# Optimization experiments

Hardware: AMD Instinct MI355X
Metric: run time of the kernel (lower is better)

## Reference

```python
import jax, jax.numpy as jnp
import numpy as np

N, E = 50000, 800000
IN, HID, H1, H2, OUT = 128, 64, 4, 6, 121
NEG_SLOPE = 0.2


def setup_inputs() -> dict:
    key = jax.random.key(0)
    ks = jax.random.split(key, 16)
    s = 0.1  # weight init scale
    return {
        "x": jax.random.normal(ks[0], (N, IN), jnp.float32),
        "src": jax.random.randint(ks[1], (E,), 0, N),
        "dst": jax.random.randint(ks[2], (E,), 0, N),
        # conv1: in=IN, heads=H1, out=HID, concat
        "W1": jax.random.normal(ks[3], (IN, H1 * HID), jnp.float32) * s,
        "a1_src": jax.random.normal(ks[4], (H1, HID), jnp.float32) * s,
        "a1_dst": jax.random.normal(ks[5], (H1, HID), jnp.float32) * s,
        "b1": jnp.zeros((H1 * HID,), jnp.float32),
        # conv2: in=H1*HID, heads=H1, out=HID, concat, residual
        "W2": jax.random.normal(ks[6], (H1 * HID, H1 * HID), jnp.float32) * s,
        "a2_src": jax.random.normal(ks[7], (H1, HID), jnp.float32) * s,
        "a2_dst": jax.random.normal(ks[8], (H1, HID), jnp.float32) * s,
        "b2": jnp.zeros((H1 * HID,), jnp.float32),
        "Wres2": jax.random.normal(ks[9], (H1 * HID, H1 * HID), jnp.float32) * s,
        # conv3: in=H1*HID, heads=H2, out=OUT, mean (concat=False)
        "W3": jax.random.normal(ks[10], (H1 * HID, H2 * OUT), jnp.float32) * s,
        "a3_src": jax.random.normal(ks[11], (H2, OUT), jnp.float32) * s,
        "a3_dst": jax.random.normal(ks[12], (H2, OUT), jnp.float32) * s,
        "b3": jnp.zeros((OUT,), jnp.float32),
    }


def _segment_softmax(e, seg, n):
    # e: [E, H], softmax over edges sharing the same destination node
    m = jax.ops.segment_max(e, seg, num_segments=n)
    ex = jnp.exp(e - m[seg])
    s = jax.ops.segment_sum(ex, seg, num_segments=n)
    return ex / (s[seg] + 1e-16)


def _gat_conv(x, src, dst, W, a_src, a_dst, b, heads, ch, concat, Wres=None):
    n = x.shape[0]
    h = (x @ W).reshape(n, heads, ch)                       # [N, H, C]
    al_s = jnp.sum(h * a_src, axis=-1)                      # [N, H]
    al_d = jnp.sum(h * a_dst, axis=-1)                      # [N, H]
    e = jax.nn.leaky_relu(al_s[src] + al_d[dst], NEG_SLOPE)  # [E, H]
    alpha = _segment_softmax(e, dst, n)                     # [E, H]
    msg = h[src] * alpha[..., None]                         # [E, H, C]
    out = jax.ops.segment_sum(msg, dst, num_segments=n)     # [N, H, C]
    out = out.reshape(n, heads * ch) if concat else out.mean(axis=1)
    if Wres is not None:
        out = out + x @ Wres
    return out + b


def reference(x, src, dst, W1, a1_src, a1_dst, b1, W2, a2_src, a2_dst, b2,
              Wres2, W3, a3_src, a3_dst, b3):
    n = x.shape[0]
    # PyG GATConv default: add self-loops
    loop = jnp.arange(n, dtype=src.dtype)
    s = jnp.concatenate([src, loop])
    d = jnp.concatenate([dst, loop])
    h = jax.nn.elu(_gat_conv(x, s, d, W1, a1_src, a1_dst, b1, H1, HID, True))
    h = jax.nn.elu(_gat_conv(h, s, d, W2, a2_src, a2_dst, b2, H1, HID, True, Wres=Wres2))
    h = _gat_conv(h, s, d, W3, a3_src, a3_dst, b3, H2, OUT, False)
    return jax.nn.sigmoid(h)
```

## Files before the change

kernel.cpp:

```cpp
#include <hip/hip_runtime.h>
#include <hip/hip_bf16.h>


#define NODES 50000
#define EDGES 800000
#define MPAD  50048
#define C0    25088
#define C1    24912

typedef unsigned short u16;
typedef __attribute__((ext_vector_type(8))) short bf16x8;
typedef __attribute__((ext_vector_type(4))) float f32x4;

__device__ __forceinline__ float bf16f(u16 r) {
    return __uint_as_float(((unsigned)r) << 16);
}
__device__ __forceinline__ u16 f2b(float v) {
    __hip_bfloat16 b = __float2bfloat16(v);
    return *(u16*)&b;
}
__device__ __forceinline__ float blo(unsigned d) { return __uint_as_float(d << 16); }
__device__ __forceinline__ float bhi(unsigned d) { return __uint_as_float(d & 0xffff0000u); }


__global__ void fill_ones_kernel(int* __restrict__ deg, int n) {
    int i = blockIdx.x * blockDim.x + threadIdx.x;
    if (i < n) deg[i] = 1;
}

__global__ void hist_kernel(const int* __restrict__ dst, int* __restrict__ deg, int E) {
    int e = blockIdx.x * blockDim.x + threadIdx.x;
    if (e < E) atomicAdd(&deg[dst[e]], 1);
}

__global__ void deg_bsum_kernel(const int* __restrict__ deg, int* __restrict__ bsum, int n) {
    int tid = threadIdx.x, lane = tid & 63, wid = tid >> 6;
    int i = blockIdx.x * 256 + tid;
    int v = (i < n) ? deg[i] : 0;
    #pragma unroll
    for (int ofs = 32; ofs > 0; ofs >>= 1) v += __shfl_down(v, ofs);
    __shared__ int sp[4];
    if (lane == 0) sp[wid] = v;
    __syncthreads();
    if (tid == 0) bsum[blockIdx.x] = sp[0] + sp[1] + sp[2] + sp[3];
}

__global__ void bsum_scan_kernel(int* __restrict__ bsum, int* __restrict__ row_ptr,
                                 int nb, int n) {
    int tid = threadIdx.x, lane = tid & 63, wid = tid >> 6;
    int v = (tid < nb) ? bsum[tid] : 0;
    int incl = v;
    #pragma unroll
    for (int ofs = 1; ofs < 64; ofs <<= 1) {
        int t = __shfl_up(incl, ofs);
        if (lane >= ofs) incl += t;
    }
    __shared__ int sp[4];
    if (lane == 63) sp[wid] = incl;
    __syncthreads();
    int add = 0;
    for (int k = 0; k < wid; k++) add += sp[k];
    int excl = incl - v + add;
    if (tid < nb) bsum[tid] = excl;
    if (tid == nb - 1) row_ptr[n] = excl + v;
}

__global__ void deg_scan_kernel(const int* __restrict__ deg, const int* __restrict__ bofs,
                                int* __restrict__ row_ptr, int* __restrict__ cursor, int n) {
    int tid = threadIdx.x, lane = tid & 63, wid = tid >> 6;
    int i = blockIdx.x * 256 + tid;
    int v = (i < n) ? deg[i] : 0;
    int incl = v;
    #pragma unroll
    for (int ofs = 1; ofs < 64; ofs <<= 1) {
        int t = __shfl_up(incl, ofs);
        if (lane >= ofs) incl += t;
    }
    __shared__ int sp[4];
    if (lane == 63) sp[wid] = incl;
    __syncthreads();
    int add = bofs[blockIdx.x];
    for (int k = 0; k < wid; k++) add += sp[k];
    int excl = incl - v + add;
    if (i < n) { row_ptr[i] = excl; cursor[i] = excl; }
}

__global__ void scatter_kernel(const int* __restrict__ src, const int* __restrict__ dst,
                               int E, int n, int* __restrict__ cursor, int* __restrict__ csr_src) {
    int e = blockIdx.x * blockDim.x + threadIdx.x;
    if (e < E) {
        int d = dst[e];
        int p = atomicAdd(&cursor[d], 1);
        csr_src[p] = src[e];
    } else if (e < E + n) {
        int i = e - E;
        int p = atomicAdd(&cursor[i], 1);
        csr_src[p] = i;
    }
}


__global__ void prep_weights(
    const float* __restrict__ W1, const float* __restrict__ W2,
    const float* __restrict__ Wres2, const float* __restrict__ W3,
    const float* __restrict__ a1s, const float* __restrict__ a1d,
    const float* __restrict__ a2s, const float* __restrict__ a2d,
    const float* __restrict__ a3s, const float* __restrict__ a3d,
    u16* __restrict__ WT1, u16* __restrict__ WT2, u16* __restrict__ W3sT,
    float* __restrict__ q1t, float* __restrict__ q2t, float* __restrict__ cm) {
    int idx = blockIdx.x * 256 + threadIdx.x;
    if (idx < 32768) {
        int n = idx >> 7, k = idx & 127;
        WT1[idx] = f2b(W1[(size_t)k * 256 + n]);
    } else if ((idx -= 32768) < 131072) {
        int n = idx >> 8, k = idx & 255;
        float v = (n < 256) ? W2[(size_t)k * 256 + n] : Wres2[(size_t)k * 256 + (n - 256)];
        WT2[idx] = f2b(v);
    } else if ((idx -= 131072) < 196608) {
        int n = idx / 1536, q = idx % 1536;
        int h = q >> 8, k = q & 255;
        W3sT[idx] = f2b((n < 121) ? W3[(size_t)k * 726 + h * 121 + n] : 0.f);
    } else if ((idx -= 196608) < 1024) {
        int h = idx >> 7, k = idx & 127;
        int hh = h & 3;
        const float* a = (h < 4) ? a1s : a1d;
        float v = 0.f;
        for (int c = 0; c < 64; c++) v += W1[(size_t)k * 256 + hh * 64 + c] * a[hh * 64 + c];
        q1t[idx] = v;
    } else if ((idx -= 1024) < 2048) {
        int h = idx >> 8, k = idx & 255;
        int hh = h & 3;
        const float* a = (h < 4) ? a2s : a2d;
        float v = 0.f;
        for (int c = 0; c < 64; c++) v += W2[(size_t)k * 256 + hh * 64 + c] * a[hh * 64 + c];
        q2t[idx] = v;
    } else if ((idx -= 2048) < 3072) {
        int o = idx >> 8, k = idx & 255;
        int h = (o < 6) ? o : o - 6;
        const float* a = (o < 6) ? a3s : a3d;
        float v = 0.f;
        for (int c = 0; c < 121; c++) v += W3[(size_t)k * 726 + h * 121 + c] * a[h * 121 + c];
        cm[idx] = v;
    }
}
#define PREP_TOTAL (32768 + 131072 + 196608 + 1024 + 2048 + 3072)


__global__ __launch_bounds__(256) void convx_al1(
    const float* __restrict__ x, const float* __restrict__ q1t,
    u16* __restrict__ A2a, float* __restrict__ alA, int n) {
    int wid = threadIdx.x >> 6, lane = threadIdx.x & 63;
    int i = blockIdx.x * 4 + wid;
    if (i >= n) return;
    float2 xv = *(const float2*)(x + (size_t)i * 128 + lane * 2);
    ushort2 o;
    o.x = f2b(xv.x); o.y = f2b(xv.y);
    *(ushort2*)(A2a + (size_t)i * 128 + lane * 2) = o;
    float p[8];
    #pragma unroll
    for (int h = 0; h < 8; h++) {
        float2 q = *(const float2*)(q1t + h * 128 + lane * 2);
        p[h] = xv.x * q.x + xv.y * q.y;
    }
    #pragma unroll
    for (int ofs = 1; ofs <= 32; ofs <<= 1) {
        #pragma unroll
        for (int h = 0; h < 8; h++) p[h] += __shfl_xor(p[h], ofs);
    }
    if (lane == 0) {
        *(float4*)(alA + (size_t)i * 8)     = make_float4(p[0], p[1], p[2], p[3]);
        *(float4*)(alA + (size_t)i * 8 + 4) = make_float4(p[4], p[5], p[6], p[7]);
    }
}


__global__ __launch_bounds__(256) void row_logit8(
    const u16* __restrict__ f, const float* __restrict__ q,
    float* __restrict__ al, int n) {
    int wid = threadIdx.x >> 6, lane = threadIdx.x & 63;
    int i = blockIdx.x * 4 + wid;
    if (i >= n) return;
    uint2 d = *(const uint2*)(f + (size_t)i * 256 + lane * 4);
    float v0 = blo(d.x), v1 = bhi(d.x), v2 = blo(d.y), v3 = bhi(d.y);
    float p[8];
    #pragma unroll
    for (int h = 0; h < 8; h++) {
        float4 c = *(const float4*)(q + (size_t)h * 256 + lane * 4);
        p[h] = v0 * c.x + v1 * c.y + v2 * c.z + v3 * c.w;
    }
    #pragma unroll
    for (int ofs = 1; ofs <= 32; ofs <<= 1) {
        #pragma unroll
        for (int h = 0; h < 8; h++) p[h] += __shfl_xor(p[h], ofs);
    }
    if (lane == 0) {
        *(float4*)(al + (size_t)i * 8)     = make_float4(p[0], p[1], p[2], p[3]);
        *(float4*)(al + (size_t)i * 8 + 4) = make_float4(p[4], p[5], p[6], p[7]);
    }
}

__global__ __launch_bounds__(256) void row_logit12(
    const u16* __restrict__ f, const float* __restrict__ q,
    float* __restrict__ al, int n) {
    int wid = threadIdx.x >> 6, lane = threadIdx.x & 63;
    int i = blockIdx.x * 4 + wid;
    if (i >= n) return;
    uint2 d = *(const uint2*)(f + (size_t)i * 256 + lane * 4);
    float v0 = blo(d.x), v1 = bhi(d.x), v2 = blo(d.y), v3 = bhi(d.y);
    float p[12];
    #pragma unroll
    for (int h = 0; h < 12; h++) {
        float4 c = *(const float4*)(q + (size_t)h * 256 + lane * 4);
        p[h] = v0 * c.x + v1 * c.y + v2 * c.z + v3 * c.w;
    }
    #pragma unroll
    for (int ofs = 1; ofs <= 32; ofs <<= 1) {
        #pragma unroll
        for (int h = 0; h < 12; h++) p[h] += __shfl_xor(p[h], ofs);
    }
    if (lane == 0) {
        *(float4*)(al + (size_t)i * 12)     = make_float4(p[0], p[1], p[2], p[3]);
        *(float4*)(al + (size_t)i * 12 + 4) = make_float4(p[4], p[5], p[6], p[7]);
        *(float4*)(al + (size_t)i * 12 + 8) = make_float4(p[8], p[9], p[10], p[11]);
    }
}


__global__ __launch_bounds__(256) void gemm_mfma_kernel(
    const u16* __restrict__ A, const u16* __restrict__ B,
    u16* __restrict__ Cb, u16* __restrict__ Cb2,
    int M, int Ncols, int K2, int ldc, int split) {
    __shared__ __align__(16) u16 As[128][40];
    __shared__ __align__(16) u16 Bs[128][40];
    int tid = threadIdx.x;
    int lane = tid & 63;
    int wv = tid >> 6;
    int quad = lane >> 4, lm = lane & 15;
    int wm = (wv & 1) * 64, wn = (wv >> 1) * 64;
    int bm = blockIdx.x * 128, bn = blockIdx.y * 128;

    f32x4 zero = {0.f, 0.f, 0.f, 0.f};
    f32x4 acc[4][4];
    #pragma unroll
    for (int i = 0; i < 4; i++)
        #pragma unroll
        for (int j = 0; j < 4; j++) acc[i][j] = zero;

    for (int k0 = 0; k0 < K2; k0 += 32) {
        #pragma unroll
        for (int it = 0; it < 2; ++it) {
            int chunk = tid + it * 256;
            int row = chunk >> 2, seg = chunk & 3;
            uint4 va = *(const uint4*)(A + (size_t)(bm + row) * K2 + k0 + seg * 8);
            uint4 vb = *(const uint4*)(B + (size_t)(bn + row) * K2 + k0 + seg * 8);
            *(uint4*)&As[row][seg * 8] = va;
            *(uint4*)&Bs[row][seg * 8] = vb;
        }
        __syncthreads();
        bf16x8 af[4], bfr[4];
        #pragma unroll
        for (int i = 0; i < 4; i++) af[i] = *(const bf16x8*)&As[wm + i * 16 + lm][quad * 8];
        #pragma unroll
        for (int j = 0; j < 4; j++) bfr[j] = *(const bf16x8*)&Bs[wn + j * 16 + lm][quad * 8];
        #pragma unroll
        for (int i = 0; i < 4; i++)
            #pragma unroll
            for (int j = 0; j < 4; j++)
                acc[i][j] = __builtin_amdgcn_mfma_f32_16x16x32_bf16(af[i], bfr[j], acc[i][j], 0, 0, 0);
        __syncthreads();
    }

    #pragma unroll
    for (int i = 0; i < 4; i++) {
        #pragma unroll
        for (int j = 0; j < 4; j++) {
            int col = bn + wn + j * 16 + lm;
            if (col >= Ncols) continue;
            int row_base = bm + wm + i * 16 + quad * 4;
            #pragma unroll
            for (int r = 0; r < 4; r++) {
                int row = row_base + r;
                if (row >= M) continue;
                float v = acc[i][j][r];
                if (col < split) Cb[(size_t)row * ldc + col] = f2b(v);
                else             Cb2[(size_t)row * ldc + col - split] = f2b(v);
            }
        }
    }
}


__global__ __launch_bounds__(256) void gemm_skinny64(
    const u16* __restrict__ A, const u16* __restrict__ B,
    float* __restrict__ C, const float* __restrict__ bias, int count) {
    __shared__ __align__(16) u16 As[64][40];
    __shared__ __align__(16) u16 Bs[128][40];
    int tid = threadIdx.x, lane = tid & 63, wv = tid >> 6;
    int quad = lane >> 4, lm = lane & 15;
    int bm = blockIdx.x * 64;
    int mrow = (wv >> 1) * 32, ncol = (wv & 1) * 64;
    int ar = bm + (tid >> 2);
    if (ar >= count) ar = count - 1;
    const u16* Ap = A + (size_t)ar * 1536 + (tid & 3) * 8;

    f32x4 zero = {0.f, 0.f, 0.f, 0.f};
    f32x4 acc[2][4];
    #pragma unroll
    for (int i = 0; i < 2; i++)
        #pragma unroll
        for (int j = 0; j < 4; j++) acc[i][j] = zero;

    for (int k0 = 0; k0 < 1536; k0 += 32) {
        *(uint4*)&As[tid >> 2][(tid & 3) * 8] = *(const uint4*)(Ap + k0);
        #pragma unroll
        for (int it = 0; it < 2; ++it) {
            int t = tid + it * 256;
            *(uint4*)&Bs[t >> 2][(t & 3) * 8] =
                *(const uint4*)(B + (size_t)(t >> 2) * 1536 + k0 + (t & 3) * 8);
        }
        __syncthreads();
        bf16x8 af[2], bfr[4];
        #pragma unroll
        for (int i = 0; i < 2; i++) af[i] = *(const bf16x8*)&As[mrow + i * 16 + lm][quad * 8];
        #pragma unroll
        for (int j = 0; j < 4; j++) bfr[j] = *(const bf16x8*)&Bs[ncol + j * 16 + lm][quad * 8];
        #pragma unroll
        for (int i = 0; i < 2; i++)
            #pragma unroll
            for (int j = 0; j < 4; j++)
                acc[i][j] = __builtin_amdgcn_mfma_f32_16x16x32_bf16(af[i], bfr[j], acc[i][j], 0, 0, 0);
        __syncthreads();
    }

    #pragma unroll
    for (int i = 0; i < 2; i++) {
        #pragma unroll
        for (int j = 0; j < 4; j++) {
            int col = ncol + j * 16 + lm;
            if (col >= 121) continue;
            int row_base = bm + mrow + i * 16 + quad * 4;
            #pragma unroll
            for (int r = 0; r < 4; r++) {
                int row = row_base + r;
                if (row >= count) continue;
                float v = acc[i][j][r] + bias[col];
                v = 1.f / (1.f + __expf(-v));
                C[(size_t)row * 121 + col] = v;
            }
        }
    }
}


#define ACC8(wt, dv) \
    acc[0] = fmaf(wt, blo(dv.x), acc[0]); acc[1] = fmaf(wt, bhi(dv.x), acc[1]); \
    acc[2] = fmaf(wt, blo(dv.y), acc[2]); acc[3] = fmaf(wt, bhi(dv.y), acc[3]); \
    acc[4] = fmaf(wt, blo(dv.z), acc[4]); acc[5] = fmaf(wt, bhi(dv.z), acc[5]); \
    acc[6] = fmaf(wt, blo(dv.w), acc[6]); acc[7] = fmaf(wt, bhi(dv.w), acc[7]);

__global__ __launch_bounds__(256) void agg4_fused(
    const u16* __restrict__ f, const float* __restrict__ al8,
    const int* __restrict__ row_ptr, const int* __restrict__ csr_src,
    const float* __restrict__ bias, const u16* __restrict__ resb,
    u16* __restrict__ outb, int n) {
    int wid = threadIdx.x >> 6, lane = threadIdx.x & 63;
    int i = blockIdx.x * 4 + wid;
    if (i >= n) return;
    int beg = row_ptr[i], end = row_ptr[i + 1];
    int h_st = lane >> 4;
    int el = lane & 15;
    int half = lane >> 5;
    int c8 = (lane & 31) * 8;
    int wsel = (lane & 24) << 1;
    float ald_st = al8[(size_t)i * 8 + 4 + h_st];
    float acc[8] = {};
    float S = 0.f;
    for (int base = beg; base < end; base += 16) {
        int cnt = min(16, end - base);
        int idxv = csr_src[base + min(el, cnt - 1)];
        float av = al8[(size_t)idxv * 8 + h_st] + ald_st;
        av = av > 0.f ? av : 0.2f * av;
        float ex = __expf(fminf(av, 60.f));
        int e = 0;
        for (; e + 8 <= cnt; e += 8) {
            int s0 = __shfl(idxv, e + half);
            int s1 = __shfl(idxv, e + 2 + half);
            int s2 = __shfl(idxv, e + 4 + half);
            int s3 = __shfl(idxv, e + 6 + half);
            uint4 d0 = *(const uint4*)(f + (size_t)s0 * 256 + c8);
            uint4 d1 = *(const uint4*)(f + (size_t)s1 * 256 + c8);
            uint4 d2 = *(const uint4*)(f + (size_t)s2 * 256 + c8);
            uint4 d3 = *(const uint4*)(f + (size_t)s3 * 256 + c8);
            float w0 = __shfl(ex, wsel | (e + half));
            float w1 = __shfl(ex, wsel | (e + 2 + half));
            float w2 = __shfl(ex, wsel | (e + 4 + half));
            float w3 = __shfl(ex, wsel | (e + 6 + half));
            S += (w0 + w1) + (w2 + w3);
            ACC8(w0, d0);
            ACC8(w1, d1);
            ACC8(w2, d2);
            ACC8(w3, d3);
        }
        for (; e + 4 <= cnt; e += 4) {
            int s0 = __shfl(idxv, e + half);
            int s1 = __shfl(idxv, e + 2 + half);
            uint4 d0 = *(const uint4*)(f + (size_t)s0 * 256 + c8);
            uint4 d1 = *(const uint4*)(f + (size_t)s1 * 256 + c8);
            float w0 = __shfl(ex, wsel | (e + half));
            float w1 = __shfl(ex, wsel | (e + 2 + half));
            S += w0 + w1;
            ACC8(w0, d0);
            ACC8(w1, d1);
        }
        for (; e < cnt; e += 2) {
            int ei = e + half;
            int eu = ei < cnt ? ei : e;
            int s = __shfl(idxv, eu);
            float w = __shfl(ex, wsel | eu);
            if (ei >= cnt) w = 0.f;
            S += w;
            uint4 d = *(const uint4*)(f + (size_t)s * 256 + c8);
            ACC8(w, d);
        }
    }
    #pragma unroll
    for (int k = 0; k < 8; k++) acc[k] += __shfl_xor(acc[k], 32);
    S += __shfl_xor(S, 32);
    if (half == 0) {
        float inv = 1.f / (S + 1e-16f);
        float4 b0 = *(const float4*)(bias + c8);
        float4 b1 = *(const float4*)(bias + c8 + 4);
        float v[8];
        v[0] = acc[0] * inv + b0.x; v[1] = acc[1] * inv + b0.y;
        v[2] = acc[2] * inv + b0.z; v[3] = acc[3] * inv + b0.w;
        v[4] = acc[4] * inv + b1.x; v[5] = acc[5] * inv + b1.y;
        v[6] = acc[6] * inv + b1.z; v[7] = acc[7] * inv + b1.w;
        if (resb) {
            uint4 r = *(const uint4*)(resb + (size_t)i * 256 + c8);
            v[0] += blo(r.x); v[1] += bhi(r.x); v[2] += blo(r.y); v[3] += bhi(r.y);
            v[4] += blo(r.z); v[5] += bhi(r.z); v[6] += blo(r.w); v[7] += bhi(r.w);
        }
        #pragma unroll
        for (int k = 0; k < 8; k++) v[k] = v[k] > 0.f ? v[k] : (__expf(v[k]) - 1.f);
        uint4 o;
        o.x = (unsigned)f2b(v[0]) | ((unsigned)f2b(v[1]) << 16);
        o.y = (unsigned)f2b(v[2]) | ((unsigned)f2b(v[3]) << 16);
        o.z = (unsigned)f2b(v[4]) | ((unsigned)f2b(v[5]) << 16);
        o.w = (unsigned)f2b(v[6]) | ((unsigned)f2b(v[7]) << 16);
        *(uint4*)(outb + (size_t)i * 256 + c8) = o;
    }
}


__global__ __launch_bounds__(256) void aggS_fused(
    const u16* __restrict__ x, const float* __restrict__ al3,
    const int* __restrict__ row_ptr, const int* __restrict__ csr_src,
    u16* __restrict__ S, int node0, int count) {
    __shared__ int s_i[4][16];
    __shared__ float s_w[4][96];
    int wid = threadIdx.x >> 6, lane = threadIdx.x & 63;
    int li = blockIdx.x * 4 + wid;
    if (li >= count) return;
    int i = node0 + li;
    int beg = row_ptr[i], end = row_ptr[i + 1];
    int c4 = lane * 4;
    int e16 = lane & 15;
    int hA = lane >> 4;
    int hB = 4 + (lane >> 4);
    float aldA = al3[(size_t)i * 12 + 6 + hA];
    float aldB = (lane < 32) ? al3[(size_t)i * 12 + 6 + hB] : 0.f;
    float acc[6][4] = {};
    float Ssum[6] = {};
    for (int base = beg; base < end; base += 16) {
        int cnt = min(16, end - base);
        int idxe = csr_src[base + min(e16, cnt - 1)];
        if (lane < 16) s_i[wid][lane] = idxe;
        float vA = al3[(size_t)idxe * 12 + hA] + aldA;
        vA = vA > 0.f ? vA : 0.2f * vA;
        float exA = __expf(fminf(vA, 60.f));
        if (e16 < cnt) s_w[wid][e16 * 6 + hA] = exA;
        if (lane < 32) {
            float vB = al3[(size_t)idxe * 12 + hB] + aldB;
            vB = vB > 0.f ? vB : 0.2f * vB;
            float exB = __expf(fminf(vB, 60.f));
            if (e16 < cnt) s_w[wid][e16 * 6 + hB] = exB;
        }
        int e = 0;
        for (; e + 4 <= cnt; e += 4) {
            int s0 = s_i[wid][e],     s1 = s_i[wid][e + 1];
            int s2 = s_i[wid][e + 2], s3 = s_i[wid][e + 3];
            uint2 d0 = *(const uint2*)(x + (size_t)s0 * 256 + c4);
            uint2 d1 = *(const uint2*)(x + (size_t)s1 * 256 + c4);
            uint2 d2 = *(const uint2*)(x + (size_t)s2 * 256 + c4);
            uint2 d3 = *(const uint2*)(x + (size_t)s3 * 256 + c4);
            float f00 = blo(d0.x), f01 = bhi(d0.x), f02 = blo(d0.y), f03 = bhi(d0.y);
            float f10 = blo(d1.x), f11 = bhi(d1.x), f12 = blo(d1.y), f13 = bhi(d1.y);
            float f20 = blo(d2.x), f21 = bhi(d2.x), f22 = blo(d2.y), f23 = bhi(d2.y);
            float f30 = blo(d3.x), f31 = bhi(d3.x), f32 = blo(d3.y), f33 = bhi(d3.y);
            #pragma unroll
            for (int hh = 0; hh < 6; hh++) {
                float w0 = s_w[wid][e * 6 + hh];
                float w1 = s_w[wid][(e + 1) * 6 + hh];
                float w2 = s_w[wid][(e + 2) * 6 + hh];
                float w3 = s_w[wid][(e + 3) * 6 + hh];
                Ssum[hh] += (w0 + w1) + (w2 + w3);
                acc[hh][0] = fmaf(w0, f00, acc[hh][0]);
                acc[hh][1] = fmaf(w0, f01, acc[hh][1]);
                acc[hh][2] = fmaf(w0, f02, acc[hh][2]);
                acc[hh][3] = fmaf(w0, f03, acc[hh][3]);
                acc[hh][0] = fmaf(w1, f10, acc[hh][0]);
                acc[hh][1] = fmaf(w1, f11, acc[hh][1]);
                acc[hh][2] = fmaf(w1, f12, acc[hh][2]);
                acc[hh][3] = fmaf(w1, f13, acc[hh][3]);
                acc[hh][0] = fmaf(w2, f20, acc[hh][0]);
                acc[hh][1] = fmaf(w2, f21, acc[hh][1]);
                acc[hh][2] = fmaf(w2, f22, acc[hh][2]);
                acc[hh][3] = fmaf(w2, f23, acc[hh][3]);
                acc[hh][0] = fmaf(w3, f30, acc[hh][0]);
                acc[hh][1] = fmaf(w3, f31, acc[hh][1]);
                acc[hh][2] = fmaf(w3, f32, acc[hh][2]);
                acc[hh][3] = fmaf(w3, f33, acc[hh][3]);
            }
        }
        for (; e < cnt; e++) {
            int s = s_i[wid][e];
            uint2 d = *(const uint2*)(x + (size_t)s * 256 + c4);
            float v0 = blo(d.x), v1 = bhi(d.x), v2 = blo(d.y), v3 = bhi(d.y);
            #pragma unroll
            for (int hh = 0; hh < 6; hh++) {
                float w = s_w[wid][e * 6 + hh];
                Ssum[hh] += w;
                acc[hh][0] = fmaf(w, v0, acc[hh][0]);
                acc[hh][1] = fmaf(w, v1, acc[hh][1]);
                acc[hh][2] = fmaf(w, v2, acc[hh][2]);
                acc[hh][3] = fmaf(w, v3, acc[hh][3]);
            }
        }
    }
    #pragma unroll
    for (int hh = 0; hh < 6; hh++) {
        float inv = 1.f / (6.f * (Ssum[hh] + 1e-16f));
        ushort4 o;
        o.x = f2b(acc[hh][0] * inv);
        o.y = f2b(acc[hh][1] * inv);
        o.z = f2b(acc[hh][2] * inv);
        o.w = f2b(acc[hh][3] * inv);
        *(ushort4*)(S + (size_t)li * 1536 + hh * 256 + c4) = o;
    }
}


extern "C" void kernel_launch(void* const* d_in, const int* in_sizes, int n_in,
                              void* d_out, int out_size, void* d_ws, size_t ws_size,
                              hipStream_t stream) {
    const float* x      = (const float*)d_in[0];
    const int*   src    = (const int*)d_in[1];
    const int*   dst    = (const int*)d_in[2];
    const float* W1     = (const float*)d_in[3];
    const float* a1_src = (const float*)d_in[4];
    const float* a1_dst = (const float*)d_in[5];
    const float* b1     = (const float*)d_in[6];
    const float* W2     = (const float*)d_in[7];
    const float* a2_src = (const float*)d_in[8];
    const float* a2_dst = (const float*)d_in[9];
    const float* b2     = (const float*)d_in[10];
    const float* Wres2  = (const float*)d_in[11];
    const float* W3     = (const float*)d_in[12];
    const float* a3_src = (const float*)d_in[13];
    const float* a3_dst = (const float*)d_in[14];
    const float* b3     = (const float*)d_in[15];
    float* out = (float*)d_out;

    const int N = NODES, E = EDGES;
    const int EN = E + N;
    const int NB = (N + 255) / 256;

    char* p = (char*)d_ws;
    auto alloc = [&](size_t bytes) -> char* {
        char* r = p;
        p += (bytes + 511) & ~(size_t)511;
        return r;
    };
    int*   row_ptr = (int*)alloc((size_t)(N + 1) * sizeof(int));
    int*   cursor  = (int*)alloc((size_t)N * sizeof(int));
    int*   deg     = (int*)alloc((size_t)N * sizeof(int));
    int*   bsum    = (int*)alloc(256 * sizeof(int));
    int*   csr_src = (int*)alloc((size_t)EN * sizeof(int));
    float* alA     = (float*)alloc((size_t)N * 8 * sizeof(float));
    float* alB     = (float*)alloc((size_t)N * 8 * sizeof(float));
    float* al3     = (float*)alloc((size_t)N * 12 * sizeof(float));
    float* q1t     = (float*)alloc((size_t)8 * 128 * sizeof(float));
    float* q2t     = (float*)alloc((size_t)8 * 256 * sizeof(float));
    float* cm      = (float*)alloc((size_t)12 * 256 * sizeof(float));
    u16*   WT1     = (u16*)alloc((size_t)256 * 128 * sizeof(u16));
    u16*   WT2     = (u16*)alloc((size_t)512 * 256 * sizeof(u16));
    u16*   W3sT    = (u16*)alloc((size_t)128 * 1536 * sizeof(u16));
    u16*   o2b     = (u16*)alloc((size_t)MPAD * 256 * sizeof(u16));
    const size_t A2B_B  = (size_t)MPAD * 256 * sizeof(u16);
    const size_t F1B_B  = (size_t)N * 256 * sizeof(u16);
    const size_t RESB_B = (size_t)N * 256 * sizeof(u16);
    const size_t S_B    = (size_t)C0 * 1536 * sizeof(u16);
    size_t r2_bytes = A2B_B + F1B_B + RESB_B;
    if (S_B > r2_bytes) r2_bytes = S_B;
    char* r2 = alloc(r2_bytes + 1024);
    u16* A2b  = (u16*)r2;
    u16* f1b  = (u16*)(r2 + A2B_B);
    u16* resb = (u16*)(r2 + A2B_B + F1B_B);
    u16* A2a  = (u16*)(r2 + A2B_B + F1B_B);
    u16* Sb   = (u16*)r2;
    (void)ws_size; (void)n_in; (void)in_sizes; (void)out_size;

    fill_ones_kernel<<<NB, 256, 0, stream>>>(deg, N);
    hist_kernel<<<(E + 255) / 256, 256, 0, stream>>>(dst, deg, E);
    deg_bsum_kernel<<<NB, 256, 0, stream>>>(deg, bsum, N);
    bsum_scan_kernel<<<1, 256, 0, stream>>>(bsum, row_ptr, NB, N);
    deg_scan_kernel<<<NB, 256, 0, stream>>>(deg, bsum, row_ptr, cursor, N);
    scatter_kernel<<<(E + N + 255) / 256, 256, 0, stream>>>(src, dst, E, N, cursor, csr_src);

    int nwb = (N + 3) / 4;

    prep_weights<<<(PREP_TOTAL + 255) / 256, 256, 0, stream>>>(
        W1, W2, Wres2, W3, a1_src, a1_dst, a2_src, a2_dst, a3_src, a3_dst,
        WT1, WT2, W3sT, q1t, q2t, cm);

    convx_al1<<<nwb, 256, 0, stream>>>(x, q1t, A2a, alA, N);
    {
        dim3 g(MPAD / 128, 2);
        gemm_mfma_kernel<<<g, 256, 0, stream>>>(A2a, WT1, f1b, nullptr, N, 256, 128, 256, 9999);
    }
    agg4_fused<<<nwb, 256, 0, stream>>>(f1b, alA, row_ptr, csr_src, b1, nullptr, A2b, N);
    row_logit8<<<nwb, 256, 0, stream>>>(A2b, q2t, alB, N);

    {
        dim3 g(MPAD / 128, 4);
        gemm_mfma_kernel<<<g, 256, 0, stream>>>(A2b, WT2, f1b, resb, N, 512, 256, 256, 256);
    }
    agg4_fused<<<nwb, 256, 0, stream>>>(f1b, alB, row_ptr, csr_src, b2, resb, o2b, N);
    row_logit12<<<nwb, 256, 0, stream>>>(o2b, cm, al3, N);

    {
        aggS_fused<<<(C0 + 3) / 4, 256, 0, stream>>>(o2b, al3, row_ptr, csr_src, Sb, 0, C0);
        gemm_skinny64<<<(C0 + 63) / 64, 256, 0, stream>>>(Sb, W3sT, out, b3, C0);
        aggS_fused<<<(C1 + 3) / 4, 256, 0, stream>>>(o2b, al3, row_ptr, csr_src, Sb, C0, C1);
        gemm_skinny64<<<(C1 + 63) / 64, 256, 0, stream>>>(Sb, W3sT, out + (size_t)C0 * 121, b3, C1);
    }
}
```

Baseline: 671.0 us.

## Fold layer-2 attention logits into GEMM columns and use nontemporal memory ops

Appends eight projected attention-vector columns (W2·a2) to the layer-2 weight matrix so the MFMA GEMM emits the source/destination logits directly. This removes the separate row_logit8 pass that re-read the activations. The cost is a fifth column-block of tiles that is mostly zero padding. It also adds nontemporal loads and stores on streaming buffers, and moves the aggS softmax-denominator sum out of the inner loop into a shuffle reduction held in shared memory. Computing the logits in bf16 inside the GEMM rather than fp32 may shift accuracy slightly.

Result: slower. 736.0 us (+9.7%).

```diff
diff --git a/kernel.cpp b/kernel.cpp
--- a/kernel.cpp
+++ b/kernel.cpp
@@ -11,6 +11,8 @@
 typedef unsigned short u16;
 typedef __attribute__((ext_vector_type(8))) short bf16x8;
 typedef __attribute__((ext_vector_type(4))) float f32x4;
+typedef __attribute__((ext_vector_type(4))) unsigned int uv4;
+typedef __attribute__((ext_vector_type(4))) unsigned short usv4;
 
 __device__ __forceinline__ float bf16f(u16 r) {
     return __uint_as_float(((unsigned)r) << 16);
@@ -107,16 +109,24 @@
     const float* __restrict__ a2s, const float* __restrict__ a2d,
     const float* __restrict__ a3s, const float* __restrict__ a3d,
     u16* __restrict__ WT1, u16* __restrict__ WT2, u16* __restrict__ W3sT,
-    float* __restrict__ q1t, float* __restrict__ q2t, float* __restrict__ cm) {
+    float* __restrict__ q1t, float* __restrict__ cm) {
     int idx = blockIdx.x * 256 + threadIdx.x;
     if (idx < 32768) {
         int n = idx >> 7, k = idx & 127;
         WT1[idx] = f2b(W1[(size_t)k * 256 + n]);
-    } else if ((idx -= 32768) < 131072) {
+    } else if ((idx -= 32768) < 163840) {
         int n = idx >> 8, k = idx & 255;
-        float v = (n < 256) ? W2[(size_t)k * 256 + n] : Wres2[(size_t)k * 256 + (n - 256)];
+        float v;
+        if (n < 256) v = W2[(size_t)k * 256 + n];
+        else if (n < 512) v = Wres2[(size_t)k * 256 + (n - 256)];
+        else if (n < 520) {
+            int h = n - 512, hh = h & 3;
+            const float* a = (h < 4) ? a2s : a2d;
+            v = 0.f;
+            for (int c = 0; c < 64; c++) v += W2[(size_t)k * 256 + hh * 64 + c] * a[hh * 64 + c];
+        } else v = 0.f;
         WT2[idx] = f2b(v);
-    } else if ((idx -= 131072) < 196608) {
+    } else if ((idx -= 163840) < 196608) {
         int n = idx / 1536, q = idx % 1536;
         int h = q >> 8, k = q & 255;
         W3sT[idx] = f2b((n < 121) ? W3[(size_t)k * 726 + h * 121 + n] : 0.f);
@@ -127,14 +137,7 @@
         float v = 0.f;
         for (int c = 0; c < 64; c++) v += W1[(size_t)k * 256 + hh * 64 + c] * a[hh * 64 + c];
         q1t[idx] = v;
-    } else if ((idx -= 1024) < 2048) {
-        int h = idx >> 8, k = idx & 255;
-        int hh = h & 3;
-        const float* a = (h < 4) ? a2s : a2d;
-        float v = 0.f;
-        for (int c = 0; c < 64; c++) v += W2[(size_t)k * 256 + hh * 64 + c] * a[hh * 64 + c];
-        q2t[idx] = v;
-    } else if ((idx -= 2048) < 3072) {
+    } else if ((idx -= 1024) < 3072) {
         int o = idx >> 8, k = idx & 255;
         int h = (o < 6) ? o : o - 6;
         const float* a = (o < 6) ? a3s : a3d;
@@ -143,7 +146,7 @@
         cm[idx] = v;
     }
 }
-#define PREP_TOTAL (32768 + 131072 + 196608 + 1024 + 2048 + 3072)
+#define PREP_TOTAL (32768 + 163840 + 196608 + 1024 + 3072)
 
 
 __global__ __launch_bounds__(256) void convx_al1(
@@ -174,31 +177,6 @@
 }
 
 
-__global__ __launch_bounds__(256) void row_logit8(
-    const u16* __restrict__ f, const float* __restrict__ q,
-    float* __restrict__ al, int n) {
-    int wid = threadIdx.x >> 6, lane = threadIdx.x & 63;
-    int i = blockIdx.x * 4 + wid;
-    if (i >= n) return;
-    uint2 d = *(const uint2*)(f + (size_t)i * 256 + lane * 4);
-    float v0 = blo(d.x), v1 = bhi(d.x), v2 = blo(d.y), v3 = bhi(d.y);
-    float p[8];
-    #pragma unroll
-    for (int h = 0; h < 8; h++) {
-        float4 c = *(const float4*)(q + (size_t)h * 256 + lane * 4);
-        p[h] = v0 * c.x + v1 * c.y + v2 * c.z + v3 * c.w;
-    }
-    #pragma unroll
-    for (int ofs = 1; ofs <= 32; ofs <<= 1) {
-        #pragma unroll
-        for (int h = 0; h < 8; h++) p[h] += __shfl_xor(p[h], ofs);
-    }
-    if (lane == 0) {
-        *(float4*)(al + (size_t)i * 8)     = make_float4(p[0], p[1], p[2], p[3]);
-        *(float4*)(al + (size_t)i * 8 + 4) = make_float4(p[4], p[5], p[6], p[7]);
-    }
-}
-
 __global__ __launch_bounds__(256) void row_logit12(
     const u16* __restrict__ f, const float* __restrict__ q,
     float* __restrict__ al, int n) {
@@ -228,8 +206,8 @@
 
 __global__ __launch_bounds__(256) void gemm_mfma_kernel(
     const u16* __restrict__ A, const u16* __restrict__ B,
-    u16* __restrict__ Cb, u16* __restrict__ Cb2,
-    int M, int Ncols, int K2, int ldc, int split) {
+    u16* __restrict__ Cb, u16* __restrict__ Cb2, float* __restrict__ alout,
+    int M, int Ncols, int K2, int ldc, int split, int logit0) {
     __shared__ __align__(16) u16 As[128][40];
     __shared__ __align__(16) u16 Bs[128][40];
     int tid = threadIdx.x;
@@ -282,8 +260,12 @@
                 int row = row_base + r;
                 if (row >= M) continue;
                 float v = acc[i][j][r];
-                if (col < split) Cb[(size_t)row * ldc + col] = f2b(v);
-                else             Cb2[(size_t)row * ldc + col - split] = f2b(v);
+                if (col < split)
+                    __builtin_nontemporal_store(f2b(v), &Cb[(size_t)row * ldc + col]);
+                else if (col < logit0)
+                    __builtin_nontemporal_store(f2b(v), &Cb2[(size_t)row * ldc + col - split]);
+                else
+                    alout[(size_t)row * 8 + (col - logit0)] = v;
             }
         }
     }
@@ -311,7 +293,8 @@
         for (int j = 0; j < 4; j++) acc[i][j] = zero;
 
     for (int k0 = 0; k0 < 1536; k0 += 32) {
-        *(uint4*)&As[tid >> 2][(tid & 3) * 8] = *(const uint4*)(Ap + k0);
+        uv4 av = __builtin_nontemporal_load((const uv4*)(Ap + k0));
+        *(uv4*)&As[tid >> 2][(tid & 3) * 8] = av;
         #pragma unroll
         for (int it = 0; it < 2; ++it) {
             int t = tid + it * 256;
@@ -345,7 +328,7 @@
                 if (row >= count) continue;
                 float v = acc[i][j][r] + bias[col];
                 v = 1.f / (1.f + __expf(-v));
-                C[(size_t)row * 121 + col] = v;
+                __builtin_nontemporal_store(v, &C[(size_t)row * 121 + col]);
             }
         }
     }
@@ -377,7 +360,7 @@
     float S = 0.f;
     for (int base = beg; base < end; base += 16) {
         int cnt = min(16, end - base);
-        int idxv = csr_src[base + min(el, cnt - 1)];
+        int idxv = __builtin_nontemporal_load(&csr_src[base + min(el, cnt - 1)]);
         float av = al8[(size_t)idxv * 8 + h_st] + ald_st;
         av = av > 0.f ? av : 0.2f * av;
         float ex = __expf(fminf(av, 60.f));
@@ -436,18 +419,18 @@
         v[4] = acc[4] * inv + b1.x; v[5] = acc[5] * inv + b1.y;
         v[6] = acc[6] * inv + b1.z; v[7] = acc[7] * inv + b1.w;
         if (resb) {
-            uint4 r = *(const uint4*)(resb + (size_t)i * 256 + c8);
+            uv4 r = __builtin_nontemporal_load((const uv4*)(resb + (size_t)i * 256 + c8));
             v[0] += blo(r.x); v[1] += bhi(r.x); v[2] += blo(r.y); v[3] += bhi(r.y);
             v[4] += blo(r.z); v[5] += bhi(r.z); v[6] += blo(r.w); v[7] += bhi(r.w);
         }
         #pragma unroll
         for (int k = 0; k < 8; k++) v[k] = v[k] > 0.f ? v[k] : (__expf(v[k]) - 1.f);
-        uint4 o;
+        uv4 o;
         o.x = (unsigned)f2b(v[0]) | ((unsigned)f2b(v[1]) << 16);
         o.y = (unsigned)f2b(v[2]) | ((unsigned)f2b(v[3]) << 16);
         o.z = (unsigned)f2b(v[4]) | ((unsigned)f2b(v[5]) << 16);
         o.w = (unsigned)f2b(v[6]) | ((unsigned)f2b(v[7]) << 16);
-        *(uint4*)(outb + (size_t)i * 256 + c8) = o;
+        __builtin_nontemporal_store(o, (uv4*)(outb + (size_t)i * 256 + c8));
     }
 }
 
@@ -458,6 +441,7 @@
     u16* __restrict__ S, int node0, int count) {
     __shared__ int s_i[4][16];
     __shared__ float s_w[4][96];
+    __shared__ float s_sum[4][6];
     int wid = threadIdx.x >> 6, lane = threadIdx.x & 63;
     int li = blockIdx.x * 4 + wid;
     if (li >= count) return;
@@ -470,20 +454,31 @@
     float aldA = al3[(size_t)i * 12 + 6 + hA];
     float aldB = (lane < 32) ? al3[(size_t)i * 12 + 6 + hB] : 0.f;
     float acc[6][4] = {};
-    float Ssum[6] = {};
+    if (lane < 6) s_sum[wid][lane] = 0.f;
     for (int base = beg; base < end; base += 16) {
         int cnt = min(16, end - base);
-        int idxe = csr_src[base + min(e16, cnt - 1)];
+        int idxe = __builtin_nontemporal_load(&csr_src[base + min(e16, cnt - 1)]);
         if (lane < 16) s_i[wid][lane] = idxe;
         float vA = al3[(size_t)idxe * 12 + hA] + aldA;
         vA = vA > 0.f ? vA : 0.2f * vA;
         float exA = __expf(fminf(vA, 60.f));
         if (e16 < cnt) s_w[wid][e16 * 6 + hA] = exA;
+        float exB = 0.f;
         if (lane < 32) {
             float vB = al3[(size_t)idxe * 12 + hB] + aldB;
             vB = vB > 0.f ? vB : 0.2f * vB;
-            float exB = __expf(fminf(vB, 60.f));
+            exB = __expf(fminf(vB, 60.f));
             if (e16 < cnt) s_w[wid][e16 * 6 + hB] = exB;
+        }
+        float sA = (e16 < cnt) ? exA : 0.f;
+        sA += __shfl_xor(sA, 1); sA += __shfl_xor(sA, 2);
+        sA += __shfl_xor(sA, 4); sA += __shfl_xor(sA, 8);
+        float sB = (lane < 32 && e16 < cnt) ? exB : 0.f;
+        sB += __shfl_xor(sB, 1); sB += __shfl_xor(sB, 2);
+        sB += __shfl_xor(sB, 4); sB += __shfl_xor(sB, 8);
+        if (e16 == 0) {
+            s_sum[wid][hA] += sA;
+            if (lane < 32) s_sum[wid][hB] += sB;
         }
         int e = 0;
         for (; e + 4 <= cnt; e += 4) {
@@ -503,7 +498,6 @@
                 float w1 = s_w[wid][(e + 1) * 6 + hh];
                 float w2 = s_w[wid][(e + 2) * 6 + hh];
                 float w3 = s_w[wid][(e + 3) * 6 + hh];
-                Ssum[hh] += (w0 + w1) + (w2 + w3);
                 acc[hh][0] = fmaf(w0, f00, acc[hh][0]);
                 acc[hh][1] = fmaf(w0, f01, acc[hh][1]);
                 acc[hh][2] = fmaf(w0, f02, acc[hh][2]);
@@ -529,7 +523,6 @@
             #pragma unroll
             for (int hh = 0; hh < 6; hh++) {
                 float w = s_w[wid][e * 6 + hh];
-                Ssum[hh] += w;
                 acc[hh][0] = fmaf(w, v0, acc[hh][0]);
                 acc[hh][1] = fmaf(w, v1, acc[hh][1]);
                 acc[hh][2] = fmaf(w, v2, acc[hh][2]);
@@ -539,13 +532,13 @@
     }
     #pragma unroll
     for (int hh = 0; hh < 6; hh++) {
-        float inv = 1.f / (6.f * (Ssum[hh] + 1e-16f));
-        ushort4 o;
+        float inv = 1.f / (6.f * (s_sum[wid][hh] + 1e-16f));
+        usv4 o;
         o.x = f2b(acc[hh][0] * inv);
         o.y = f2b(acc[hh][1] * inv);
         o.z = f2b(acc[hh][2] * inv);
         o.w = f2b(acc[hh][3] * inv);
-        *(ushort4*)(S + (size_t)li * 1536 + hh * 256 + c4) = o;
+        __builtin_nontemporal_store(o, (usv4*)(S + (size_t)li * 1536 + hh * 256 + c4));
     }
 }
 
@@ -590,10 +583,9 @@
     float* alB     = (float*)alloc((size_t)N * 8 * sizeof(float));
     float* al3     = (float*)alloc((size_t)N * 12 * sizeof(float));
     float* q1t     = (float*)alloc((size_t)8 * 128 * sizeof(float));
-    float* q2t     = (float*)alloc((size_t)8 * 256 * sizeof(float));
     float* cm      = (float*)alloc((size_t)12 * 256 * sizeof(float));
     u16*   WT1     = (u16*)alloc((size_t)256 * 128 * sizeof(u16));
-    u16*   WT2     = (u16*)alloc((size_t)512 * 256 * sizeof(u16));
+    u16*   WT2     = (u16*)alloc((size_t)640 * 256 * sizeof(u16));
     u16*   W3sT    = (u16*)alloc((size_t)128 * 1536 * sizeof(u16));
     u16*   o2b     = (u16*)alloc((size_t)MPAD * 256 * sizeof(u16));
     const size_t A2B_B  = (size_t)MPAD * 256 * sizeof(u16);
@@ -621,19 +613,20 @@
 
     prep_weights<<<(PREP_TOTAL + 255) / 256, 256, 0, stream>>>(
         W1, W2, Wres2, W3, a1_src, a1_dst, a2_src, a2_dst, a3_src, a3_dst,
-        WT1, WT2, W3sT, q1t, q2t, cm);
+        WT1, WT2, W3sT, q1t, cm);
 
     convx_al1<<<nwb, 256, 0, stream>>>(x, q1t, A2a, alA, N);
     {
         dim3 g(MPAD / 128, 2);
-        gemm_mfma_kernel<<<g, 256, 0, stream>>>(A2a, WT1, f1b, nullptr, N, 256, 128, 256, 9999);
+        gemm_mfma_kernel<<<g, 256, 0, stream>>>(A2a, WT1, f1b, nullptr, nullptr,
+                                                N, 256, 128, 256, 9999, 10000);
     }
     agg4_fused<<<nwb, 256, 0, stream>>>(f1b, alA, row_ptr, csr_src, b1, nullptr, A2b, N);
-    row_logit8<<<nwb, 256, 0, stream>>>(A2b, q2t, alB, N);
 
     {
-        dim3 g(MPAD / 128, 4);
-        gemm_mfma_kernel<<<g, 256, 0, stream>>>(A2b, WT2, f1b, resb, N, 512, 256, 256, 256);
+        dim3 g(MPAD / 128, 5);
+        gemm_mfma_kernel<<<g, 256, 0, stream>>>(A2b, WT2, f1b, resb, alB,
+                                                N, 520, 256, 256, 256, 512);
     }
     agg4_fused<<<nwb, 256, 0, stream>>>(f1b, alB, row_ptr, csr_src, b2, resb, o2b, N);
     row_logit12<<<nwb, 256, 0, stream>>>(o2b, cm, al3, N);
```
